# Kernel tuning notes

Hardware: AMD Instinct MI355X
Metric: run time of the kernel (lower is better)

## Reference

```python
import jax, jax.numpy as jnp
import numpy as np

WS = 8        # window_size
SHIFT = 4     # shift_size
NH = 6        # num_heads
EPS = 1e-5


def _rel_pos_index(ws):
    coords = np.stack(np.meshgrid(np.arange(ws), np.arange(ws), indexing='ij'))  # [2,ws,ws]
    cf = coords.reshape(2, -1)                      # [2, ws*ws]
    rel = cf[:, :, None] - cf[:, None, :]           # [2, N, N]
    rel = rel.transpose(1, 2, 0)                    # [N, N, 2]
    rel[:, :, 0] += ws - 1
    rel[:, :, 1] += ws - 1
    rel[:, :, 0] *= 2 * ws - 1
    return rel.sum(-1)                              # [N, N] int


def _attn_mask(H, W, ws, shift):
    img = np.zeros((H, W), dtype=np.float32)
    slices = (slice(0, -ws), slice(-ws, -shift), slice(-shift, None))
    cnt = 0
    for hs in slices:
        for wsl in slices:
            img[hs, wsl] = cnt
            cnt += 1
    mw = img.reshape(H // ws, ws, W // ws, ws).transpose(0, 2, 1, 3).reshape(-1, ws * ws)
    diff = mw[:, None, :] - mw[:, :, None]          # [nW, N, N]
    return np.where(diff != 0, -100.0, 0.0).astype(np.float32)


def _layernorm(x, g, b):
    mu = x.mean(-1, keepdims=True)
    var = ((x - mu) ** 2).mean(-1, keepdims=True)
    return (x - mu) * jax.lax.rsqrt(var + EPS) * g + b


def setup_inputs() -> dict:
    key = jax.random.key(0)
    ks = jax.random.split(key, 8)
    C, HID = 192, 768
    return {
        'x': jax.random.normal(ks[0], (8, 128, 128, C), jnp.float32),
        'g1': jnp.ones((C,), jnp.float32),
        'b1': jnp.zeros((C,), jnp.float32),
        'qkv_w': jax.random.normal(ks[1], (3 * C, C), jnp.float32) * 0.02,
        'qkv_b': jnp.zeros((3 * C,), jnp.float32),
        'rpb_table': jax.random.normal(ks[2], ((2 * WS - 1) ** 2, NH), jnp.float32) * 0.02,
        'proj_w': jax.random.normal(ks[3], (C, C), jnp.float32) * 0.02,
        'proj_b': jnp.zeros((C,), jnp.float32),
        'g2': jnp.ones((C,), jnp.float32),
        'b2': jnp.zeros((C,), jnp.float32),
        'fc1_w': jax.random.normal(ks[4], (HID, C), jnp.float32) * 0.02,
        'fc1_b': jnp.zeros((HID,), jnp.float32),
        'fc2_w': jax.random.normal(ks[5], (C, HID), jnp.float32) * 0.02,
        'fc2_b': jnp.zeros((C,), jnp.float32),
    }


def reference(x, g1, b1, qkv_w, qkv_b, rpb_table, proj_w, proj_b, g2, b2,
              fc1_w, fc1_b, fc2_w, fc2_b):
    B, H, W, C = x.shape
    N = WS * WS
    hd = C // NH
    scale = hd ** -0.5

    rpi = jnp.asarray(_rel_pos_index(WS))                 # [N,N] static
    mask = jnp.asarray(_attn_mask(H, W, WS, SHIFT))       # [nW,N,N] static
    nW = mask.shape[0]

    shortcut = x.reshape(B, H * W, C)
    xn = _layernorm(shortcut, g1, b1).reshape(B, H, W, C)

    # cyclic shift
    xs = jnp.roll(xn, shift=(-SHIFT, -SHIFT), axis=(1, 2))

    # window partition -> [B*nW, N, C]
    win = xs.reshape(B, H // WS, WS, W // WS, WS, C).transpose(0, 1, 3, 2, 4, 5)
    win = win.reshape(-1, N, C)
    B_ = win.shape[0]

    # qkv
    qkv = jnp.einsum('bnc,oc->bno', win, qkv_w) + qkv_b   # [B_,N,3C]
    qkv = qkv.reshape(B_, N, 3, NH, hd).transpose(2, 0, 3, 1, 4)  # [3,B_,NH,N,hd]
    q, k, v = qkv[0] * scale, qkv[1], qkv[2]

    attn = jnp.einsum('bhnd,bhmd->bhnm', q, k)            # [B_,NH,N,N]
    bias = rpb_table[rpi.reshape(-1)].reshape(N, N, NH).transpose(2, 0, 1)
    attn = attn + bias[None]
    attn = attn.reshape(B, nW, NH, N, N) + mask[None, :, None]
    attn = jax.nn.softmax(attn.reshape(B_, NH, N, N), axis=-1)

    out = jnp.einsum('bhnm,bhmd->bhnd', attn, v)          # [B_,NH,N,hd]
    out = out.transpose(0, 2, 1, 3).reshape(B_, N, C)
    out = jnp.einsum('bnc,oc->bno', out, proj_w) + proj_b

    # window reverse -> [B,H,W,C]
    out = out.reshape(B, H // WS, W // WS, WS, WS, C).transpose(0, 1, 3, 2, 4, 5)
    out = out.reshape(B, H, W, C)
    out = jnp.roll(out, shift=(SHIFT, SHIFT), axis=(1, 2)).reshape(B, H * W, C)

    x1 = shortcut + out
    h = _layernorm(x1, g2, b2)
    h = jnp.einsum('bnc,hc->bnh', h, fc1_w) + fc1_b
    h = jax.nn.gelu(h, approximate=False)
    h = jnp.einsum('bnh,ch->bnc', h, fc2_w) + fc2_b
    x2 = x1 + h
    return x2.reshape(B, H, W, C)
```

## Files before the change

### kernel.cpp

```cpp
#include <hip/hip_runtime.h>
#include <hip/hip_bf16.h>

typedef __attribute__((ext_vector_type(8))) short s16x8;
typedef __attribute__((ext_vector_type(4))) float f32x4;

__device__ __forceinline__ unsigned short f2bf(float f){
    __hip_bfloat16 h = __float2bfloat16(f);
    return *reinterpret_cast<unsigned short*>(&h);
}

__device__ __forceinline__ int flab(int g){ return (g < 120) ? 0 : ((g < 124) ? 1 : 2); }

__device__ __forceinline__ void async16(const void* g, void* l){
    __builtin_amdgcn_global_load_lds(
        (const __attribute__((address_space(1))) unsigned int*)g,
        (__attribute__((address_space(3))) unsigned int*)l, 16, 0, 0);
}

__global__ __launch_bounds__(256) void wconv_all(
    const float* __restrict__ w0, const float* __restrict__ w1,
    const float* __restrict__ w2, const float* __restrict__ w3,
    unsigned short* __restrict__ o0, unsigned short* __restrict__ o1,
    unsigned short* __restrict__ o2, unsigned short* __restrict__ o3)
{
    int i = blockIdx.x*256 + threadIdx.x;
    if (i < 110592) o0[i] = f2bf(w0[i]);
    if (i < 36864)  o1[i] = f2bf(w1[i]);
    if (i < 147456) o2[i] = f2bf(w2[i]);
    if (i < 147456) o3[i] = f2bf(w3[i]);
}

__global__ __launch_bounds__(256) void lnqkv_kernel(
    const float* __restrict__ x, const float* __restrict__ g1, const float* __restrict__ b1,
    const unsigned short* __restrict__ wq, const float* __restrict__ qkvb,
    unsigned short* __restrict__ qo, unsigned short* __restrict__ ko,
    unsigned short* __restrict__ vo)
{
    __shared__ __attribute__((aligned(16))) unsigned short win[64*200];
    __shared__ __attribute__((aligned(16))) unsigned short Bs[64*200];
    const int b_ = blockIdx.x;
    const int bb = b_>>8, wi = b_&255, wh = wi>>4, ww = wi&15;
    const int tid = threadIdx.x;
    const int wv = tid>>6, lane = tid&63, lrow = lane&15, quad = lane>>4;

    {
        const int n = tid>>2, q4 = tid&3;
        const int r = n>>3, c = n&7;
        const int hh = (wh*8 + r + 4)&127, wp = (ww*8 + c + 4)&127;
        const float* px = x + (((size_t)bb*128+hh)*128+wp)*192 + q4*48;
        float v[48];
        #pragma unroll
        for (int m=0;m<12;++m) *(float4*)(v+m*4) = *(const float4*)(px+m*4);
        float s = 0.f;
        #pragma unroll
        for (int k=0;k<48;++k) s += v[k];
        s += __shfl_xor(s,1); s += __shfl_xor(s,2);
        float mu = s*(1.0f/192.0f);
        float qv = 0.f;
        #pragma unroll
        for (int k=0;k<48;++k){ float d=v[k]-mu; qv += d*d; }
        qv += __shfl_xor(qv,1); qv += __shfl_xor(qv,2);
        float rstd = rsqrtf(qv*(1.0f/192.0f) + 1e-5f);
        const float* pg = g1 + q4*48;
        const float* pb = b1 + q4*48;
        unsigned short* pw = win + n*200 + q4*48;
        #pragma unroll
        for (int k=0;k<48;++k) pw[k] = f2bf((v[k]-mu)*rstd*pg[k] + pb[k]);
    }
    __syncthreads();

    s16x8 af[6];
    #pragma unroll
    for (int kc=0;kc<6;++kc)
        af[kc] = *(const s16x8*)(win + (wv*16+lrow)*200 + kc*32 + quad*8);

    for (int ot=0; ot<9; ++ot) {
        const int o0 = ot*64;
        __syncthreads();
        #pragma unroll
        for (int t=0;t<6;++t) {
            int cid = tid + t*256;
            *(int4*)(Bs + (cid/24)*200 + (cid%24)*8) =
                *(const int4*)(wq + (size_t)o0*192 + cid*8);
        }
        __syncthreads();
        f32x4 acc[4];
        #pragma unroll
        for (int j=0;j<4;++j) acc[j] = (f32x4){0.f,0.f,0.f,0.f};
        #pragma unroll
        for (int kc=0;kc<6;++kc)
            #pragma unroll
            for (int j=0;j<4;++j) {
                s16x8 bf = *(const s16x8*)(Bs + (j*16+lrow)*200 + kc*32 + quad*8);
                acc[j] = __builtin_amdgcn_mfma_f32_16x16x32_bf16(af[kc], bf, acc[j], 0, 0, 0);
            }
        __syncthreads();
        unsigned short* T = Bs;
        const int part = ot/3;
        float bv[4];
        #pragma unroll
        for (int j=0;j<4;++j) bv[j] = qkvb[o0 + j*16 + lrow];

        if (part < 2) {
            const float scale = (part==0) ? 0.17677669529663687f : 1.0f;
            #pragma unroll
            for (int j=0;j<4;++j)
                #pragma unroll
                for (int rg=0;rg<4;++rg) {
                    int n2 = wv*16 + quad*4 + rg;
                    T[n2*72 + j*16 + lrow] = f2bf((acc[j][rg]+bv[j])*scale);
                }
            __syncthreads();
            unsigned short* dst = (part==0) ? qo : ko;
            #pragma unroll
            for (int t=0;t<2;++t) {
                int c = tid + t*256;
                int n2 = c>>3, blk = c&7;
                int o_in = o0 + blk*8 - part*192;
                int head = o_in>>5, d = o_in&31;
                *(int4*)(dst + (((size_t)b_*6+head)*64 + n2)*32 + d) =
                    *(const int4*)(T + n2*72 + blk*8);
            }
        } else {
            #pragma unroll
            for (int j=0;j<4;++j)
                #pragma unroll
                for (int rg=0;rg<4;++rg) {
                    int n2 = wv*16 + quad*4 + rg;
                    T[(j*16+lrow)*72 + n2] = f2bf(acc[j][rg]+bv[j]);
                }
            __syncthreads();
            #pragma unroll
            for (int t=0;t<2;++t) {
                int c = tid + t*256;
                int ol = c>>3, nb = (c&7)*8;
                int o_in = o0 + ol - 384;
                int head = o_in>>5, d = o_in&31;
                *(int4*)(vo + (((size_t)b_*6+head)*32 + d)*64 + nb) =
                    *(const int4*)(T + ol*72 + nb);
            }
        }
    }
}

__global__ __launch_bounds__(384) void attn_kernel(
    const unsigned short* __restrict__ q, const unsigned short* __restrict__ k,
    const unsigned short* __restrict__ vT, const float* __restrict__ rpb,
    unsigned short* __restrict__ ao)
{
    __shared__ float rpb_s[1350];
    __shared__ __attribute__((aligned(16))) unsigned short p_lds[6*4608];
    const int b_ = blockIdx.x;
    const int h = threadIdx.x >> 6;
    const int lane = threadIdx.x & 63, lrow = lane & 15, quad = lane >> 4;
    for (int i = threadIdx.x; i < 1350; i += 384) rpb_s[i] = rpb[i];
    __syncthreads();

    const size_t hb = ((size_t)b_*6 + h)*2048;
    const unsigned short* qb = q  + hb;
    const unsigned short* kb = k  + hb;
    const unsigned short* vb = vT + hb;

    s16x8 qf[4], kf[4];
    #pragma unroll
    for (int i = 0; i < 4; ++i) qf[i] = *(const s16x8*)(qb + (i*16+lrow)*32 + quad*8);
    #pragma unroll
    for (int j = 0; j < 4; ++j) kf[j] = *(const s16x8*)(kb + (j*16+lrow)*32 + quad*8);

    const f32x4 zz = {0.f,0.f,0.f,0.f};
    f32x4 s[4][4];
    #pragma unroll
    for (int i = 0; i < 4; ++i)
        #pragma unroll
        for (int j = 0; j < 4; ++j)
            s[i][j] = __builtin_amdgcn_mfma_f32_16x16x32_bf16(qf[i], kf[j], zz, 0, 0, 0);

    const int wi = b_ & 255, wh = wi >> 4, ww = wi & 15;
    int labm[4];
    #pragma unroll
    for (int j = 0; j < 4; ++j) {
        int m = j*16 + lrow;
        labm[j] = flab(wh*8 + (m >> 3))*3 + flab(ww*8 + (m & 7));
    }
    unsigned short* pl = p_lds + h*4608;
    #pragma unroll
    for (int i = 0; i < 4; ++i) {
        #pragma unroll
        for (int rg = 0; rg < 4; ++rg) {
            int n = i*16 + quad*4 + rg;
            int rn = n >> 3, cn = n & 7;
            int labn = flab(wh*8 + rn)*3 + flab(ww*8 + cn);
            float vals[4];
            float vmax = -1e30f;
            #pragma unroll
            for (int j = 0; j < 4; ++j) {
                int m = j*16 + lrow;
                int idx = ((rn - (m >> 3) + 7)*15 + (cn - (m & 7) + 7))*6 + h;
                float val = s[i][j][rg] + rpb_s[idx];
                if (labn != labm[j]) val -= 100.f;
                vals[j] = val;
                vmax = fmaxf(vmax, val);
            }
            #pragma unroll
            for (int o = 1; o < 16; o <<= 1) vmax = fmaxf(vmax, __shfl_xor(vmax, o));
            float sum = 0.f;
            #pragma unroll
            for (int j = 0; j < 4; ++j) { vals[j] = __expf(vals[j] - vmax); sum += vals[j]; }
            #pragma unroll
            for (int o = 1; o < 16; o <<= 1) sum += __shfl_xor(sum, o);
            float inv = 1.f / sum;
            #pragma unroll
            for (int j = 0; j < 4; ++j) pl[n*72 + j*16 + lrow] = f2bf(vals[j]*inv);
        }
    }
    __syncthreads();

    f32x4 oacc[4][2];
    #pragma unroll
    for (int i = 0; i < 4; ++i) { oacc[i][0] = zz; oacc[i][1] = zz; }
    #pragma unroll
    for (int kc = 0; kc < 2; ++kc) {
        s16x8 vf[2];
        #pragma unroll
        for (int jd = 0; jd < 2; ++jd)
            vf[jd] = *(const s16x8*)(vb + (jd*16+lrow)*64 + kc*32 + quad*8);
        #pragma unroll
        for (int i = 0; i < 4; ++i) {
            s16x8 pf = *(const s16x8*)(pl + (i*16+lrow)*72 + kc*32 + quad*8);
            #pragma unroll
            for (int jd = 0; jd < 2; ++jd)
                oacc[i][jd] = __builtin_amdgcn_mfma_f32_16x16x32_bf16(pf, vf[jd], oacc[i][jd], 0, 0, 0);
        }
    }
    unsigned short* ob = ao + (size_t)b_*12288 + h*32;
    #pragma unroll
    for (int i = 0; i < 4; ++i)
        #pragma unroll
        for (int jd = 0; jd < 2; ++jd)
            #pragma unroll
            for (int rg = 0; rg < 4; ++rg) {
                int n = i*16 + quad*4 + rg;
                ob[(size_t)n*192 + jd*16 + lrow] = f2bf(oacc[i][jd][rg]);
            }
}

__global__ __launch_bounds__(256) void projln_kernel(
    const unsigned short* __restrict__ A, const unsigned short* __restrict__ W,
    const float* __restrict__ pbias, const float* __restrict__ x,
    const float* __restrict__ g2, const float* __restrict__ b2,
    float* __restrict__ x1, unsigned short* __restrict__ xln2)
{
    __shared__ __attribute__((aligned(16))) char smem[36864];
    unsigned short* As = (unsigned short*)smem;
    unsigned short* Bs = (unsigned short*)(smem + 9216);
    const int b_ = blockIdx.x;
    const int tid = threadIdx.x, wv = tid>>6, lane = tid&63;
    const int lrow = lane&15, quad = lane>>4;
    const size_t m0 = (size_t)b_*64;

    f32x4 acc[12];
    #pragma unroll
    for (int j=0;j<12;++j) acc[j] = (f32x4){0.f,0.f,0.f,0.f};

    for (int k0=0;k0<192;k0+=64) {
        __syncthreads();
        #pragma unroll
        for (int t=0;t<2;++t) {
            int cid = tid + t*256;
            *(int4*)(As + (cid>>3)*72 + (cid&7)*8) =
                *(const int4*)(A + (m0 + (cid>>3))*192 + k0 + (cid&7)*8);
        }
        #pragma unroll
        for (int t=0;t<6;++t) {
            int cid = tid + t*256;
            *(int4*)(Bs + (cid>>3)*72 + (cid&7)*8) =
                *(const int4*)(W + (size_t)(cid>>3)*192 + k0 + (cid&7)*8);
        }
        __syncthreads();
        #pragma unroll
        for (int kc=0;kc<2;++kc) {
            s16x8 af = *(const s16x8*)(As + (wv*16+lrow)*72 + kc*32 + quad*8);
            #pragma unroll
            for (int j=0;j<12;++j) {
                s16x8 bf = *(const s16x8*)(Bs + (j*16+lrow)*72 + kc*32 + quad*8);
                acc[j] = __builtin_amdgcn_mfma_f32_16x16x32_bf16(af, bf, acc[j], 0, 0, 0);
            }
        }
    }
    __syncthreads();

    const int bb = b_>>8, wi = b_&255, wh = wi>>4, ww = wi&15;
    float bv[12], gv[12], b2v[12];
    #pragma unroll
    for (int j=0;j<12;++j) {
        bv[j]  = pbias[j*16+lrow];
        gv[j]  = g2[j*16+lrow];
        b2v[j] = b2[j*16+lrow];
    }
    unsigned short* T = (unsigned short*)smem;
    #pragma unroll
    for (int rg=0;rg<4;++rg) {
        int n2 = wv*16 + quad*4 + rg;
        int r = n2>>3, c = n2&7;
        int hh = (wh*8+r+4)&127, wp = (ww*8+c+4)&127;
        size_t tok = ((size_t)bb*128+hh)*128 + wp;
        float xv[12];
        float s = 0.f;
        #pragma unroll
        for (int j=0;j<12;++j) {
            float t = acc[j][rg] + bv[j] + x[tok*192 + j*16 + lrow];
            xv[j] = t; s += t;
        }
        #pragma unroll
        for (int o=1;o<16;o<<=1) s += __shfl_xor(s, o);
        float mu = s*(1.0f/192.0f);
        float qv = 0.f;
        #pragma unroll
        for (int j=0;j<12;++j){ float d = xv[j]-mu; qv += d*d; }
        #pragma unroll
        for (int o=1;o<16;o<<=1) qv += __shfl_xor(qv, o);
        float rstd = rsqrtf(qv*(1.0f/192.0f) + 1e-5f);
        #pragma unroll
        for (int j=0;j<12;++j) {
            x1[tok*192 + j*16 + lrow] = xv[j];
            T[n2*200 + j*16 + lrow] = f2bf((xv[j]-mu)*rstd*gv[j] + b2v[j]);
        }
    }
    __syncthreads();
    #pragma unroll
    for (int t=0;t<6;++t) {
        int cid = tid + t*256;
        int n2 = cid/24, blk = cid%24;
        int r = n2>>3, c = n2&7;
        int hh = (wh*8+r+4)&127, wp = (ww*8+c+4)&127;
        size_t tok = ((size_t)bb*128+hh)*128 + wp;
        *(int4*)(xln2 + tok*192 + blk*8) = *(const int4*)(T + n2*200 + blk*8);
    }
}

__device__ __forceinline__ void mm128x64(
    const unsigned short* __restrict__ A, const unsigned short* __restrict__ W,
    int K, size_t m0, int o0, unsigned short* As, unsigned short* Bs,
    f32x4 (&acc)[2][4])
{
    const int tid = threadIdx.x, wv = tid>>6, lane = tid&63;
    const int lrow = lane&15, quad = lane>>4;
    const int lr8 = lane>>3, lb = lane&7;
    const int sb = ((lb ^ lr8) << 3);
    #pragma unroll
    for (int i=0;i<2;++i)
        #pragma unroll
        for (int j=0;j<4;++j) acc[i][j] = (f32x4){0.f,0.f,0.f,0.f};

    const unsigned short* Abase = A + (m0 + wv*8 + lr8)*K + sb;
    const unsigned short* Wbase = W + (size_t)(o0 + wv*8 + lr8)*K + sb;

    for (int k0=0;k0<K;k0+=64) {
        #pragma unroll
        for (int it=0;it<4;++it)
            async16(Abase + (size_t)(it*32)*K + k0, As + (it*4+wv)*512);
        #pragma unroll
        for (int it=0;it<2;++it)
            async16(Wbase + (size_t)(it*32)*K + k0, Bs + (it*4+wv)*512);
        __syncthreads();
        #pragma unroll
        for (int kc=0;kc<2;++kc) {
            const int blk = quad + 4*kc;
            s16x8 af[2], bf[4];
            #pragma unroll
            for (int i=0;i<2;++i) {
                int row = wv*32 + i*16 + lrow;
                af[i] = *(const s16x8*)(As + row*64 + ((blk ^ (row&7)) << 3));
            }
            #pragma unroll
            for (int j=0;j<4;++j) {
                int row = j*16 + lrow;
                bf[j] = *(const s16x8*)(Bs + row*64 + ((blk ^ (row&7)) << 3));
            }
            #pragma unroll
            for (int i=0;i<2;++i)
                #pragma unroll
                for (int j=0;j<4;++j)
                    acc[i][j] = __builtin_amdgcn_mfma_f32_16x16x32_bf16(af[i], bf[j], acc[i][j], 0, 0, 0);
        }
        __syncthreads();
    }
}

__global__ __launch_bounds__(256) void gemm_fc1_kernel(
    const unsigned short* __restrict__ A, const unsigned short* __restrict__ Wm,
    const float* __restrict__ bias, unsigned short* __restrict__ h1)
{
    __shared__ __attribute__((aligned(16))) char smem[24576];
    unsigned short* As = (unsigned short*)smem;
    unsigned short* Bs = (unsigned short*)(smem + 16384);
    const size_t m0 = (size_t)blockIdx.y*128;
    const int o0 = blockIdx.x*64;
    f32x4 acc[2][4];
    mm128x64(A, Wm, 192, m0, o0, As, Bs, acc);
    const int tid = threadIdx.x, wv = tid>>6, lane = tid&63;
    const int lrow = lane&15, quad = lane>>4;
    float bv[4];
    #pragma unroll
    for (int j=0;j<4;++j) bv[j] = bias[o0 + j*16 + lrow];
    unsigned short* T = (unsigned short*)smem;
    #pragma unroll
    for (int i=0;i<2;++i)
        #pragma unroll
        for (int j=0;j<4;++j)
            #pragma unroll
            for (int rg=0;rg<4;++rg) {
                int ml = wv*32 + i*16 + quad*4 + rg;
                float v = acc[i][j][rg] + bv[j];
                v = 0.5f*v*(1.0f + erff(v*0.7071067811865475f));
                T[ml*72 + j*16 + lrow] = f2bf(v);
            }
    __syncthreads();
    #pragma unroll
    for (int t=0;t<4;++t) {
        int c = tid + t*256;
        int row = c>>3, blk = c&7;
        *(int4*)(h1 + (m0+row)*768 + o0 + blk*8) = *(const int4*)(T + row*72 + blk*8);
    }
}

__global__ __launch_bounds__(256) void gemm_fc2_kernel(
    const unsigned short* __restrict__ A, const unsigned short* __restrict__ Wm,
    const float* __restrict__ bias, const float* __restrict__ x1, float* __restrict__ out)
{
    __shared__ __attribute__((aligned(16))) char smem[24576];
    unsigned short* As = (unsigned short*)smem;
    unsigned short* Bs = (unsigned short*)(smem + 16384);
    const size_t m0 = (size_t)blockIdx.y*128;
    const int o0 = blockIdx.x*64;
    f32x4 acc[2][4];
    mm128x64(A, Wm, 768, m0, o0, As, Bs, acc);
    const int tid = threadIdx.x, wv = tid>>6, lane = tid&63;
    const int lrow = lane&15, quad = lane>>4;
    float bv[4];
    #pragma unroll
    for (int j=0;j<4;++j) bv[j] = bias[o0 + j*16 + lrow];
    float* T = (float*)smem;
    #pragma unroll
    for (int p=0;p<2;++p) {
        __syncthreads();
        if ((wv>>1) == p) {
            int wl = wv&1;
            #pragma unroll
            for (int i=0;i<2;++i)
                #pragma unroll
                for (int j=0;j<4;++j)
                    #pragma unroll
                    for (int rg=0;rg<4;++rg)
                        T[(wl*32 + i*16 + quad*4 + rg)*68 + j*16 + lrow] = acc[i][j][rg] + bv[j];
        }
        __syncthreads();
        #pragma unroll
        for (int t=0;t<4;++t) {
            int c = tid + t*256;
            int row = c>>4, blk = c&15;
            size_t ad = (m0 + p*64 + row)*192 + o0 + blk*4;
            float4 v = *(const float4*)(T + row*68 + blk*4);
            float4 rx = *(const float4*)(x1 + ad);
            v.x += rx.x; v.y += rx.y; v.z += rx.z; v.w += rx.w;
            *(float4*)(out + ad) = v;
        }
    }
}

extern "C" void kernel_launch(void* const* d_in, const int* in_sizes, int n_in,
                              void* d_out, int out_size, void* d_ws, size_t ws_size,
                              hipStream_t stream)
{
    const float* x      = (const float*)d_in[0];
    const float* g1     = (const float*)d_in[1];
    const float* b1     = (const float*)d_in[2];
    const float* qkv_w  = (const float*)d_in[3];
    const float* qkv_b  = (const float*)d_in[4];
    const float* rpb    = (const float*)d_in[5];
    const float* proj_w = (const float*)d_in[6];
    const float* proj_b = (const float*)d_in[7];
    const float* g2     = (const float*)d_in[8];
    const float* b2     = (const float*)d_in[9];
    const float* fc1_w  = (const float*)d_in[10];
    const float* fc1_b  = (const float*)d_in[11];
    const float* fc2_w  = (const float*)d_in[12];
    const float* fc2_b  = (const float*)d_in[13];
    float* out = (float*)d_out;
    char* ws = (char*)d_ws;

    if (ws_size < 353206272ULL) return;

    unsigned short* qbuf  = (unsigned short*)(ws + 0);
    unsigned short* kbuf  = (unsigned short*)(ws + 50331648);
    unsigned short* vbuf  = (unsigned short*)(ws + 100663296);
    unsigned short* attnO = (unsigned short*)(ws + 150994944);
    float*          x1    = (float*)        (ws + 201326592);
    unsigned short* xln2  = (unsigned short*)(ws + 301989888);
    unsigned short* wq    = (unsigned short*)(ws + 352321536);
    unsigned short* wp    = (unsigned short*)(ws + 352321536 + 221184);
    unsigned short* w1    = (unsigned short*)(ws + 352321536 + 221184 + 73728);
    unsigned short* w2    = (unsigned short*)(ws + 352321536 + 221184 + 73728 + 294912);
    unsigned short* h1    = (unsigned short*)(ws + 0);

    wconv_all<<<576, 256, 0, stream>>>(qkv_w, proj_w, fc1_w, fc2_w, wq, wp, w1, w2);
    lnqkv_kernel<<<2048, 256, 0, stream>>>(x, g1, b1, wq, qkv_b, qbuf, kbuf, vbuf);
    attn_kernel<<<2048, 384, 0, stream>>>(qbuf, kbuf, vbuf, rpb, attnO);
    projln_kernel<<<2048, 256, 0, stream>>>(attnO, wp, proj_b, x, g2, b2, x1, xln2);
    gemm_fc1_kernel<<<dim3(12, 1024), 256, 0, stream>>>(xln2, w1, fc1_b, h1);
    gemm_fc2_kernel<<<dim3(3, 1024), 256, 0, stream>>>(h1, w2, fc2_b, x1, out);
}
```

Baseline: 591.3 us.

## Read weights directly from global in GEMMs and swap MFMA operands to drop LDS staging

Result: slower. 1.066 ms (+80.2%).

```diff
diff --git a/kernel.cpp b/kernel.cpp
--- a/kernel.cpp
+++ b/kernel.cpp
@@ -11,10 +11,11 @@
 
 __device__ __forceinline__ int flab(int g){ return (g < 120) ? 0 : ((g < 124) ? 1 : 2); }
 
-__device__ __forceinline__ void async16(const void* g, void* l){
-    __builtin_amdgcn_global_load_lds(
-        (const __attribute__((address_space(1))) unsigned int*)g,
-        (__attribute__((address_space(3))) unsigned int*)l, 16, 0, 0);
+__device__ __forceinline__ uint2 pack4(float a, float b, float c, float d){
+    uint2 r;
+    r.x = (unsigned)f2bf(a) | ((unsigned)f2bf(b) << 16);
+    r.y = (unsigned)f2bf(c) | ((unsigned)f2bf(d) << 16);
+    return r;
 }
 
 __global__ __launch_bounds__(256) void wconv_all(
@@ -37,7 +38,7 @@
     unsigned short* __restrict__ vo)
 {
     __shared__ __attribute__((aligned(16))) unsigned short win[64*200];
-    __shared__ __attribute__((aligned(16))) unsigned short Bs[64*200];
+    __shared__ __attribute__((aligned(16))) unsigned short T[64*72];
     const int b_ = blockIdx.x;
     const int bb = b_>>8, wi = b_&255, wh = wi>>4, ww = wi&15;
     const int tid = threadIdx.x;
@@ -46,8 +47,8 @@
     {
         const int n = tid>>2, q4 = tid&3;
         const int r = n>>3, c = n&7;
-        const int hh = (wh*8 + r + 4)&127, wp = (ww*8 + c + 4)&127;
-        const float* px = x + (((size_t)bb*128+hh)*128+wp)*192 + q4*48;
+        const int hh = (wh*8 + r + 4)&127, wp2 = (ww*8 + c + 4)&127;
+        const float* px = x + (((size_t)bb*128+hh)*128+wp2)*192 + q4*48;
         float v[48];
         #pragma unroll
         for (int m=0;m<12;++m) *(float4*)(v+m*4) = *(const float4*)(px+m*4);
@@ -69,21 +70,14 @@
     }
     __syncthreads();
 
-    s16x8 af[6];
+    s16x8 bfr[6];
     #pragma unroll
     for (int kc=0;kc<6;++kc)
-        af[kc] = *(const s16x8*)(win + (wv*16+lrow)*200 + kc*32 + quad*8);
+        bfr[kc] = *(const s16x8*)(win + (wv*16+lrow)*200 + kc*32 + quad*8);
+    const int token = wv*16 + lrow;
 
     for (int ot=0; ot<9; ++ot) {
         const int o0 = ot*64;
-        __syncthreads();
-        #pragma unroll
-        for (int t=0;t<6;++t) {
-            int cid = tid + t*256;
-            *(int4*)(Bs + (cid/24)*200 + (cid%24)*8) =
-                *(const int4*)(wq + (size_t)o0*192 + cid*8);
-        }
-        __syncthreads();
         f32x4 acc[4];
         #pragma unroll
         for (int j=0;j<4;++j) acc[j] = (f32x4){0.f,0.f,0.f,0.f};
@@ -91,54 +85,45 @@
         for (int kc=0;kc<6;++kc)
             #pragma unroll
             for (int j=0;j<4;++j) {
-                s16x8 bf = *(const s16x8*)(Bs + (j*16+lrow)*200 + kc*32 + quad*8);
-                acc[j] = __builtin_amdgcn_mfma_f32_16x16x32_bf16(af[kc], bf, acc[j], 0, 0, 0);
-            }
-        __syncthreads();
-        unsigned short* T = Bs;
+                s16x8 af = *(const s16x8*)(wq + (size_t)(o0 + j*16 + lrow)*192 + kc*32 + quad*8);
+                acc[j] = __builtin_amdgcn_mfma_f32_16x16x32_bf16(af, bfr[kc], acc[j], 0, 0, 0);
+            }
         const int part = ot/3;
-        float bv[4];
-        #pragma unroll
-        for (int j=0;j<4;++j) bv[j] = qkvb[o0 + j*16 + lrow];
-
         if (part < 2) {
+            unsigned short* dst = (part==0) ? qo : ko;
             const float scale = (part==0) ? 0.17677669529663687f : 1.0f;
             #pragma unroll
-            for (int j=0;j<4;++j)
-                #pragma unroll
-                for (int rg=0;rg<4;++rg) {
-                    int n2 = wv*16 + quad*4 + rg;
-                    T[n2*72 + j*16 + lrow] = f2bf((acc[j][rg]+bv[j])*scale);
-                }
+            for (int j=0;j<4;++j) {
+                int o = o0 + j*16 + quad*4;
+                float4 bv = *(const float4*)(qkvb + o);
+                int o_in = o - part*192;
+                int head = o_in>>5, d = o_in&31;
+                uint2 pk = pack4((acc[j][0]+bv.x)*scale, (acc[j][1]+bv.y)*scale,
+                                 (acc[j][2]+bv.z)*scale, (acc[j][3]+bv.w)*scale);
+                *(uint2*)(dst + (((size_t)b_*6+head)*64 + token)*32 + d) = pk;
+            }
+        } else {
+            #pragma unroll
+            for (int j=0;j<4;++j) {
+                int o = o0 + j*16 + quad*4;
+                float4 bv = *(const float4*)(qkvb + o);
+                int ol = j*16 + quad*4;
+                T[(ol+0)*72 + token] = f2bf(acc[j][0]+bv.x);
+                T[(ol+1)*72 + token] = f2bf(acc[j][1]+bv.y);
+                T[(ol+2)*72 + token] = f2bf(acc[j][2]+bv.z);
+                T[(ol+3)*72 + token] = f2bf(acc[j][3]+bv.w);
+            }
             __syncthreads();
-            unsigned short* dst = (part==0) ? qo : ko;
-            #pragma unroll
-            for (int t=0;t<2;++t) {
-                int c = tid + t*256;
-                int n2 = c>>3, blk = c&7;
-                int o_in = o0 + blk*8 - part*192;
-                int head = o_in>>5, d = o_in&31;
-                *(int4*)(dst + (((size_t)b_*6+head)*64 + n2)*32 + d) =
-                    *(const int4*)(T + n2*72 + blk*8);
-            }
-        } else {
-            #pragma unroll
-            for (int j=0;j<4;++j)
-                #pragma unroll
-                for (int rg=0;rg<4;++rg) {
-                    int n2 = wv*16 + quad*4 + rg;
-                    T[(j*16+lrow)*72 + n2] = f2bf(acc[j][rg]+bv[j]);
-                }
-            __syncthreads();
-            #pragma unroll
-            for (int t=0;t<2;++t) {
-                int c = tid + t*256;
+            #pragma unroll
+            for (int tt=0;tt<2;++tt) {
+                int c = tid + tt*256;
                 int ol = c>>3, nb = (c&7)*8;
                 int o_in = o0 + ol - 384;
                 int head = o_in>>5, d = o_in&31;
                 *(int4*)(vo + (((size_t)b_*6+head)*32 + d)*64 + nb) =
                     *(const int4*)(T + ol*72 + nb);
             }
+            __syncthreads();
         }
     }
 }
@@ -250,220 +235,152 @@
     const float* __restrict__ g2, const float* __restrict__ b2,
     float* __restrict__ x1, unsigned short* __restrict__ xln2)
 {
-    __shared__ __attribute__((aligned(16))) char smem[36864];
-    unsigned short* As = (unsigned short*)smem;
-    unsigned short* Bs = (unsigned short*)(smem + 9216);
     const int b_ = blockIdx.x;
     const int tid = threadIdx.x, wv = tid>>6, lane = tid&63;
     const int lrow = lane&15, quad = lane>>4;
-    const size_t m0 = (size_t)b_*64;
+    const int n2 = wv*16 + lrow;
+    const size_t m = (size_t)b_*64 + n2;
+
+    s16x8 bfr[6];
+    #pragma unroll
+    for (int kc=0;kc<6;++kc)
+        bfr[kc] = *(const s16x8*)(A + m*192 + kc*32 + quad*8);
 
     f32x4 acc[12];
     #pragma unroll
     for (int j=0;j<12;++j) acc[j] = (f32x4){0.f,0.f,0.f,0.f};
-
-    for (int k0=0;k0<192;k0+=64) {
-        __syncthreads();
-        #pragma unroll
-        for (int t=0;t<2;++t) {
-            int cid = tid + t*256;
-            *(int4*)(As + (cid>>3)*72 + (cid&7)*8) =
-                *(const int4*)(A + (m0 + (cid>>3))*192 + k0 + (cid&7)*8);
-        }
-        #pragma unroll
-        for (int t=0;t<6;++t) {
-            int cid = tid + t*256;
-            *(int4*)(Bs + (cid>>3)*72 + (cid&7)*8) =
-                *(const int4*)(W + (size_t)(cid>>3)*192 + k0 + (cid&7)*8);
-        }
-        __syncthreads();
-        #pragma unroll
-        for (int kc=0;kc<2;++kc) {
-            s16x8 af = *(const s16x8*)(As + (wv*16+lrow)*72 + kc*32 + quad*8);
-            #pragma unroll
-            for (int j=0;j<12;++j) {
-                s16x8 bf = *(const s16x8*)(Bs + (j*16+lrow)*72 + kc*32 + quad*8);
-                acc[j] = __builtin_amdgcn_mfma_f32_16x16x32_bf16(af, bf, acc[j], 0, 0, 0);
-            }
-        }
-    }
-    __syncthreads();
+    #pragma unroll
+    for (int kc=0;kc<6;++kc)
+        #pragma unroll
+        for (int j=0;j<12;++j) {
+            s16x8 af = *(const s16x8*)(W + (size_t)(j*16 + lrow)*192 + kc*32 + quad*8);
+            acc[j] = __builtin_amdgcn_mfma_f32_16x16x32_bf16(af, bfr[kc], acc[j], 0, 0, 0);
+        }
 
     const int bb = b_>>8, wi = b_&255, wh = wi>>4, ww = wi&15;
-    float bv[12], gv[12], b2v[12];
+    const int r = n2>>3, c = n2&7;
+    const int hh = (wh*8+r+4)&127, wp2 = (ww*8+c+4)&127;
+    const size_t tok = ((size_t)bb*128+hh)*128 + wp2;
+
+    float xv[12][4];
+    float s = 0.f;
     #pragma unroll
     for (int j=0;j<12;++j) {
-        bv[j]  = pbias[j*16+lrow];
-        gv[j]  = g2[j*16+lrow];
-        b2v[j] = b2[j*16+lrow];
-    }
-    unsigned short* T = (unsigned short*)smem;
-    #pragma unroll
-    for (int rg=0;rg<4;++rg) {
-        int n2 = wv*16 + quad*4 + rg;
-        int r = n2>>3, c = n2&7;
-        int hh = (wh*8+r+4)&127, wp = (ww*8+c+4)&127;
-        size_t tok = ((size_t)bb*128+hh)*128 + wp;
-        float xv[12];
-        float s = 0.f;
-        #pragma unroll
-        for (int j=0;j<12;++j) {
-            float t = acc[j][rg] + bv[j] + x[tok*192 + j*16 + lrow];
-            xv[j] = t; s += t;
-        }
-        #pragma unroll
-        for (int o=1;o<16;o<<=1) s += __shfl_xor(s, o);
-        float mu = s*(1.0f/192.0f);
-        float qv = 0.f;
-        #pragma unroll
-        for (int j=0;j<12;++j){ float d = xv[j]-mu; qv += d*d; }
-        #pragma unroll
-        for (int o=1;o<16;o<<=1) qv += __shfl_xor(qv, o);
-        float rstd = rsqrtf(qv*(1.0f/192.0f) + 1e-5f);
-        #pragma unroll
-        for (int j=0;j<12;++j) {
-            x1[tok*192 + j*16 + lrow] = xv[j];
-            T[n2*200 + j*16 + lrow] = f2bf((xv[j]-mu)*rstd*gv[j] + b2v[j]);
-        }
-    }
-    __syncthreads();
-    #pragma unroll
-    for (int t=0;t<6;++t) {
-        int cid = tid + t*256;
-        int n2 = cid/24, blk = cid%24;
-        int r = n2>>3, c = n2&7;
-        int hh = (wh*8+r+4)&127, wp = (ww*8+c+4)&127;
-        size_t tok = ((size_t)bb*128+hh)*128 + wp;
-        *(int4*)(xln2 + tok*192 + blk*8) = *(const int4*)(T + n2*200 + blk*8);
-    }
-}
-
-__device__ __forceinline__ void mm128x64(
+        int o = j*16 + quad*4;
+        float4 bv = *(const float4*)(pbias + o);
+        float4 rx = *(const float4*)(x + tok*192 + o);
+        xv[j][0] = acc[j][0]+bv.x+rx.x; xv[j][1] = acc[j][1]+bv.y+rx.y;
+        xv[j][2] = acc[j][2]+bv.z+rx.z; xv[j][3] = acc[j][3]+bv.w+rx.w;
+        s += xv[j][0]+xv[j][1]+xv[j][2]+xv[j][3];
+    }
+    s += __shfl_xor(s,16); s += __shfl_xor(s,32);
+    float mu = s*(1.0f/192.0f);
+    float qv = 0.f;
+    #pragma unroll
+    for (int j=0;j<12;++j)
+        #pragma unroll
+        for (int rg=0;rg<4;++rg){ float d = xv[j][rg]-mu; qv += d*d; }
+    qv += __shfl_xor(qv,16); qv += __shfl_xor(qv,32);
+    float rstd = rsqrtf(qv*(1.0f/192.0f) + 1e-5f);
+    #pragma unroll
+    for (int j=0;j<12;++j) {
+        int o = j*16 + quad*4;
+        *(float4*)(x1 + tok*192 + o) = *(const float4*)(xv[j]);
+        float4 gv = *(const float4*)(g2 + o);
+        float4 b2v = *(const float4*)(b2 + o);
+        uint2 pk = pack4((xv[j][0]-mu)*rstd*gv.x + b2v.x, (xv[j][1]-mu)*rstd*gv.y + b2v.y,
+                         (xv[j][2]-mu)*rstd*gv.z + b2v.z, (xv[j][3]-mu)*rstd*gv.w + b2v.w);
+        *(uint2*)(xln2 + tok*192 + o) = pk;
+    }
+}
+
+__global__ __launch_bounds__(256) void gemm_fc1_kernel(
     const unsigned short* __restrict__ A, const unsigned short* __restrict__ W,
-    int K, size_t m0, int o0, unsigned short* As, unsigned short* Bs,
-    f32x4 (&acc)[2][4])
+    const float* __restrict__ bias, unsigned short* __restrict__ h1)
 {
     const int tid = threadIdx.x, wv = tid>>6, lane = tid&63;
     const int lrow = lane&15, quad = lane>>4;
-    const int lr8 = lane>>3, lb = lane&7;
-    const int sb = ((lb ^ lr8) << 3);
-    #pragma unroll
-    for (int i=0;i<2;++i)
-        #pragma unroll
-        for (int j=0;j<4;++j) acc[i][j] = (f32x4){0.f,0.f,0.f,0.f};
-
-    const unsigned short* Abase = A + (m0 + wv*8 + lr8)*K + sb;
-    const unsigned short* Wbase = W + (size_t)(o0 + wv*8 + lr8)*K + sb;
-
-    for (int k0=0;k0<K;k0+=64) {
-        #pragma unroll
-        for (int it=0;it<4;++it)
-            async16(Abase + (size_t)(it*32)*K + k0, As + (it*4+wv)*512);
-        #pragma unroll
-        for (int it=0;it<2;++it)
-            async16(Wbase + (size_t)(it*32)*K + k0, Bs + (it*4+wv)*512);
-        __syncthreads();
-        #pragma unroll
-        for (int kc=0;kc<2;++kc) {
-            const int blk = quad + 4*kc;
-            s16x8 af[2], bf[4];
-            #pragma unroll
-            for (int i=0;i<2;++i) {
-                int row = wv*32 + i*16 + lrow;
-                af[i] = *(const s16x8*)(As + row*64 + ((blk ^ (row&7)) << 3));
-            }
-            #pragma unroll
-            for (int j=0;j<4;++j) {
-                int row = j*16 + lrow;
-                bf[j] = *(const s16x8*)(Bs + row*64 + ((blk ^ (row&7)) << 3));
-            }
-            #pragma unroll
-            for (int i=0;i<2;++i)
-                #pragma unroll
-                for (int j=0;j<4;++j)
-                    acc[i][j] = __builtin_amdgcn_mfma_f32_16x16x32_bf16(af[i], bf[j], acc[i][j], 0, 0, 0);
-        }
-        __syncthreads();
-    }
-}
-
-__global__ __launch_bounds__(256) void gemm_fc1_kernel(
-    const unsigned short* __restrict__ A, const unsigned short* __restrict__ Wm,
-    const float* __restrict__ bias, unsigned short* __restrict__ h1)
-{
-    __shared__ __attribute__((aligned(16))) char smem[24576];
-    unsigned short* As = (unsigned short*)smem;
-    unsigned short* Bs = (unsigned short*)(smem + 16384);
-    const size_t m0 = (size_t)blockIdx.y*128;
-    const int o0 = blockIdx.x*64;
-    f32x4 acc[2][4];
-    mm128x64(A, Wm, 192, m0, o0, As, Bs, acc);
+    const size_t m0 = (size_t)blockIdx.x*128;
+
+    s16x8 bfr[2][6];
+    #pragma unroll
+    for (int t=0;t<2;++t)
+        #pragma unroll
+        for (int kc=0;kc<6;++kc)
+            bfr[t][kc] = *(const s16x8*)(A + (m0 + wv*32 + t*16 + lrow)*192 + kc*32 + quad*8);
+
+    for (int oc=0; oc<8; ++oc) {
+        f32x4 acc[2][6];
+        #pragma unroll
+        for (int t=0;t<2;++t)
+            #pragma unroll
+            for (int j=0;j<6;++j) acc[t][j] = (f32x4){0.f,0.f,0.f,0.f};
+        #pragma unroll
+        for (int kc=0;kc<6;++kc)
+            #pragma unroll
+            for (int j=0;j<6;++j) {
+                s16x8 af = *(const s16x8*)(W + (size_t)(oc*96 + j*16 + lrow)*192 + kc*32 + quad*8);
+                acc[0][j] = __builtin_amdgcn_mfma_f32_16x16x32_bf16(af, bfr[0][kc], acc[0][j], 0, 0, 0);
+                acc[1][j] = __builtin_amdgcn_mfma_f32_16x16x32_bf16(af, bfr[1][kc], acc[1][j], 0, 0, 0);
+            }
+        #pragma unroll
+        for (int t=0;t<2;++t) {
+            size_t token = m0 + wv*32 + t*16 + lrow;
+            #pragma unroll
+            for (int j=0;j<6;++j) {
+                int o = oc*96 + j*16 + quad*4;
+                float4 bv = *(const float4*)(bias + o);
+                float v0 = acc[t][j][0]+bv.x, v1 = acc[t][j][1]+bv.y;
+                float v2 = acc[t][j][2]+bv.z, v3 = acc[t][j][3]+bv.w;
+                v0 = 0.5f*v0*(1.0f+erff(v0*0.7071067811865475f));
+                v1 = 0.5f*v1*(1.0f+erff(v1*0.7071067811865475f));
+                v2 = 0.5f*v2*(1.0f+erff(v2*0.7071067811865475f));
+                v3 = 0.5f*v3*(1.0f+erff(v3*0.7071067811865475f));
+                *(uint2*)(h1 + token*768 + o) = pack4(v0,v1,v2,v3);
+            }
+        }
+    }
+}
+
+__global__ __launch_bounds__(256) void gemm_fc2_kernel(
+    const unsigned short* __restrict__ A, const unsigned short* __restrict__ W,
+    const float* __restrict__ bias, const float* __restrict__ x1, float* __restrict__ out)
+{
     const int tid = threadIdx.x, wv = tid>>6, lane = tid&63;
     const int lrow = lane&15, quad = lane>>4;
-    float bv[4];
-    #pragma unroll
-    for (int j=0;j<4;++j) bv[j] = bias[o0 + j*16 + lrow];
-    unsigned short* T = (unsigned short*)smem;
-    #pragma unroll
-    for (int i=0;i<2;++i)
-        #pragma unroll
-        for (int j=0;j<4;++j)
-            #pragma unroll
-            for (int rg=0;rg<4;++rg) {
-                int ml = wv*32 + i*16 + quad*4 + rg;
-                float v = acc[i][j][rg] + bv[j];
-                v = 0.5f*v*(1.0f + erff(v*0.7071067811865475f));
-                T[ml*72 + j*16 + lrow] = f2bf(v);
-            }
-    __syncthreads();
-    #pragma unroll
-    for (int t=0;t<4;++t) {
-        int c = tid + t*256;
-        int row = c>>3, blk = c&7;
-        *(int4*)(h1 + (m0+row)*768 + o0 + blk*8) = *(const int4*)(T + row*72 + blk*8);
-    }
-}
-
-__global__ __launch_bounds__(256) void gemm_fc2_kernel(
-    const unsigned short* __restrict__ A, const unsigned short* __restrict__ Wm,
-    const float* __restrict__ bias, const float* __restrict__ x1, float* __restrict__ out)
-{
-    __shared__ __attribute__((aligned(16))) char smem[24576];
-    unsigned short* As = (unsigned short*)smem;
-    unsigned short* Bs = (unsigned short*)(smem + 16384);
-    const size_t m0 = (size_t)blockIdx.y*128;
-    const int o0 = blockIdx.x*64;
-    f32x4 acc[2][4];
-    mm128x64(A, Wm, 768, m0, o0, As, Bs, acc);
-    const int tid = threadIdx.x, wv = tid>>6, lane = tid&63;
-    const int lrow = lane&15, quad = lane>>4;
-    float bv[4];
-    #pragma unroll
-    for (int j=0;j<4;++j) bv[j] = bias[o0 + j*16 + lrow];
-    float* T = (float*)smem;
-    #pragma unroll
-    for (int p=0;p<2;++p) {
-        __syncthreads();
-        if ((wv>>1) == p) {
-            int wl = wv&1;
-            #pragma unroll
-            for (int i=0;i<2;++i)
-                #pragma unroll
-                for (int j=0;j<4;++j)
-                    #pragma unroll
-                    for (int rg=0;rg<4;++rg)
-                        T[(wl*32 + i*16 + quad*4 + rg)*68 + j*16 + lrow] = acc[i][j][rg] + bv[j];
-        }
-        __syncthreads();
-        #pragma unroll
-        for (int t=0;t<4;++t) {
-            int c = tid + t*256;
-            int row = c>>4, blk = c&15;
-            size_t ad = (m0 + p*64 + row)*192 + o0 + blk*4;
-            float4 v = *(const float4*)(T + row*68 + blk*4);
-            float4 rx = *(const float4*)(x1 + ad);
-            v.x += rx.x; v.y += rx.y; v.z += rx.z; v.w += rx.w;
-            *(float4*)(out + ad) = v;
+    const size_t m0 = (size_t)blockIdx.x*128;
+
+    f32x4 acc[2][12];
+    #pragma unroll
+    for (int t=0;t<2;++t)
+        #pragma unroll
+        for (int j=0;j<12;++j) acc[t][j] = (f32x4){0.f,0.f,0.f,0.f};
+
+    #pragma unroll
+    for (int kc=0;kc<24;++kc) {
+        s16x8 bt[2];
+        #pragma unroll
+        for (int t=0;t<2;++t)
+            bt[t] = *(const s16x8*)(A + (m0 + wv*32 + t*16 + lrow)*768 + kc*32 + quad*8);
+        #pragma unroll
+        for (int j=0;j<12;++j) {
+            s16x8 af = *(const s16x8*)(W + (size_t)(j*16 + lrow)*768 + kc*32 + quad*8);
+            acc[0][j] = __builtin_amdgcn_mfma_f32_16x16x32_bf16(af, bt[0], acc[0][j], 0, 0, 0);
+            acc[1][j] = __builtin_amdgcn_mfma_f32_16x16x32_bf16(af, bt[1], acc[1][j], 0, 0, 0);
+        }
+    }
+    #pragma unroll
+    for (int t=0;t<2;++t) {
+        size_t token = m0 + wv*32 + t*16 + lrow;
+        #pragma unroll
+        for (int j=0;j<12;++j) {
+            int o = j*16 + quad*4;
+            float4 bv = *(const float4*)(bias + o);
+            float4 rx = *(const float4*)(x1 + token*192 + o);
+            float4 v;
+            v.x = acc[t][j][0]+bv.x+rx.x; v.y = acc[t][j][1]+bv.y+rx.y;
+            v.z = acc[t][j][2]+bv.z+rx.z; v.w = acc[t][j][3]+bv.w+rx.w;
+            *(float4*)(out + token*192 + o) = v;
         }
     }
 }
@@ -507,6 +424,6 @@
     lnqkv_kernel<<<2048, 256, 0, stream>>>(x, g1, b1, wq, qkv_b, qbuf, kbuf, vbuf);
     attn_kernel<<<2048, 384, 0, stream>>>(qbuf, kbuf, vbuf, rpb, attnO);
     projln_kernel<<<2048, 256, 0, stream>>>(attnO, wp, proj_b, x, g2, b2, x1, xln2);
-    gemm_fc1_kernel<<<dim3(12, 1024), 256, 0, stream>>>(xln2, w1, fc1_b, h1);
-    gemm_fc2_kernel<<<dim3(3, 1024), 256, 0, stream>>>(h1, w2, fc2_b, x1, out);
-}
+    gemm_fc1_kernel<<<1024, 256, 0, stream>>>(xln2, w1, fc1_b, h1);
+    gemm_fc2_kernel<<<1024, 256, 0, stream>>>(h1, w2, fc2_b, x1, out);
+}
```
